# Performance work log

Measured on AMD Instinct MI355X. Metric: run time of the kernel, lower is better.

The kernel has to match this reference:

```python
import jax, jax.numpy as jnp
import numpy as np
from jax import lax

W_MAX = 8
STEP = 1
LEAK = 2
KSIZE = (W_MAX - 1) * (STEP + LEAK)  # 21 = kernel size, padding, and fodep
THETA = 80
FODEP = KSIZE
OUT_CH = 1
NEURONS = 1024


def make_w_kernel_table():
    # StepFireLeak response table: [w_max, ksize], flipped in time
    w_idx = np.arange(W_MAX, dtype=np.float32)[:, None]
    t_idx = np.arange(KSIZE, dtype=np.float32)[None, :]
    w_step = np.maximum(np.floor(1.0 + t_idx / STEP), 0.0)
    w_leak = np.maximum(np.ceil(w_idx + ((w_idx - 1.0) * STEP - t_idx) / LEAK), 0.0)
    table = np.minimum(w_step, w_leak).astype(np.int32)[:, ::-1]
    return jnp.asarray(np.ascontiguousarray(table))


def setup_inputs() -> dict:
    key = jax.random.key(0)
    k1, k2 = jax.random.split(key)
    B, C, S, T = 64, 1, 784, 500
    input_spikes = (jax.random.uniform(k1, (B, C, S, T)) < 0.05).astype(jnp.float32)
    # integer synaptic weights in [0, w_max)
    weight = jax.random.randint(k2, (OUT_CH * NEURONS, C * S), 0, W_MAX, dtype=jnp.int32)
    return {"input_spikes": input_spikes, "weight": weight}


def reference(input_spikes, weight):
    B, C, S, T = input_spikes.shape
    x = input_spikes.reshape(B, C * S, T)
    # expand integer weights into response kernels: [out, in, ksize]
    table = make_w_kernel_table().astype(jnp.float32)
    kern = table[weight]
    pot = lax.conv_general_dilated(
        x, kern, window_strides=(1,), padding=[(KSIZE, KSIZE)],
        dimension_numbers=("NCH", "OIH", "NCH"))
    pot = jnp.rint(pot).astype(jnp.int32)
    Tp = pot.shape[-1]  # T + ksize + 1
    pot = pot.reshape(B, OUT_CH, NEURONS, Tp)
    pot_t = jnp.transpose(pot, (3, 0, 1, 2))  # [Tp, B, C, N]

    def step(dep, p):  # dep: [B, C] int32, p: [B, C, N]
        winner = jnp.argmax(p, axis=-1)  # [B, C]
        val = jnp.take_along_axis(p, winner[..., None], axis=-1)[..., 0]
        cond = ((val > THETA) & (dep == 0)).astype(jnp.int32)  # min_depression == 0
        winners_t = jax.nn.one_hot(winner, NEURONS, dtype=jnp.int32) * cond[..., None]
        new_dep = jnp.maximum(0, dep + cond * (FODEP + 1) - 1)
        return new_dep, winners_t

    dep0 = jnp.zeros((B, OUT_CH), dtype=jnp.int32)
    _, winners = lax.scan(step, dep0, pot_t)  # [Tp, B, C, N]
    return jnp.transpose(winners, (1, 2, 3, 0))  # [B, C, N, Tp]
```

## Files before the change

kernel.cpp:

```cpp
#include <hip/hip_runtime.h>

#define B_DIM 64
#define S_DIM 784
#define T_DIM 500
#define N_DIM 1024
#define TP    522
#define KS    21
#define THETA 80
#define NCHUNK 8
#define CH    66
#define LISTCAP 128

__global__ void k_prep(const int* __restrict__ w, unsigned char* __restrict__ wt9,
                       unsigned* __restrict__ gcnt) {
  unsigned idx = blockIdx.x * 256 + threadIdx.x;
  if (idx < S_DIM * N_DIM) {
    unsigned s = idx >> 10, n = idx & 1023;
    int wv = w[n * S_DIM + s];
    wt9[idx] = wv ? (unsigned char)(9 * (wv - 1)) : (unsigned char)63;
  }
  if (idx < B_DIM * T_DIM) gcnt[idx] = 0;
}

__global__ void k_lists(const float* __restrict__ x, unsigned* __restrict__ gcnt,
                        unsigned short* __restrict__ glist) {
  unsigned idx = blockIdx.x * 256 + threadIdx.x;
  if (idx >= B_DIM * S_DIM * T_DIM) return;
  if (x[idx] != 0.0f) {
    unsigned t = idx % T_DIM;
    unsigned s = (idx / T_DIM) % S_DIM;
    unsigned b = idx / (S_DIM * T_DIM);
    unsigned cell = b * T_DIM + t;
    unsigned pos = atomicAdd(&gcnt[cell], 1u);
    if (pos < LISTCAP) glist[cell * LISTCAP + pos] = (unsigned short)s;
  }
}

__global__ void __launch_bounds__(1024, 8)
k_main(const unsigned char* __restrict__ wt9,
       const unsigned* __restrict__ gcnt,
       const unsigned short* __restrict__ glist,
       unsigned* __restrict__ red) {
  __shared__ unsigned short s_list[87][LISTCAP];
  __shared__ int s_cnt[87];
  __shared__ unsigned smax[CH];

  const int tid = threadIdx.x;
  const int b = blockIdx.y;
  const int lo = blockIdx.x * CH;
  const int hi = min(TP - 1, lo + CH - 1);
  const int t0 = max(0, lo - KS);
  const int n_emit = hi - lo + 1;
  const int nt_in = min(hi, T_DIM - 1) - t0 + 1;

  const unsigned cell0 = (unsigned)b * T_DIM + (unsigned)t0;
  for (int i = tid; i < nt_in; i += 1024)
    s_cnt[i] = min((int)gcnt[cell0 + i], LISTCAP);
  {
    const unsigned* src = (const unsigned*)(glist + (size_t)cell0 * LISTCAP);
    unsigned* dst = (unsigned*)&s_list[0][0];
    const int nw = nt_in * (LISTCAP / 2);
    for (int i = tid; i < nw; i += 1024) dst[i] = src[i];
  }
  for (int i = tid; i < n_emit; i += 1024) smax[i] = 0u;
  __syncthreads();

  int ring[KS + 1];
  #pragma unroll
  for (int i = 0; i <= KS; ++i) ring[i] = 0;

  const unsigned invn = (unsigned)(1023 - tid);

  for (int t = t0; t <= hi; ++t) {
    if (t >= lo) {
      unsigned key = ((unsigned)ring[0] << 10) | invn;
      #pragma unroll
      for (int off = 32; off > 0; off >>= 1) {
        unsigned o = __shfl_xor(key, off, 64);
        key = key > o ? key : o;
      }
      if ((tid & 63) == 0) atomicMax(&smax[t - lo], key);
    }

    if (t < T_DIM) {
      const int li = t - t0;
      const int cnt = __builtin_amdgcn_readfirstlane(s_cnt[li]);
      const unsigned short* lp = &s_list[li][0];
      unsigned long long ca = 0, cb = 0;
      int i = 0;
      for (; i + 1 < cnt; i += 2) {
        unsigned ia = ((unsigned)lp[i] << 10) + tid;
        unsigned ib = ((unsigned)lp[i + 1] << 10) + tid;
        ca += 1ull << wt9[ia];
        cb += 1ull << wt9[ib];
      }
      if (i < cnt) ca += 1ull << wt9[((unsigned)lp[i] << 10) + tid];
      const unsigned long long c = ca + cb;

      const int c1 = (int)(c & 511), c2 = (int)((c >> 9) & 511), c3 = (int)((c >> 18) & 511),
                c4 = (int)((c >> 27) & 511), c5 = (int)((c >> 36) & 511),
                c6 = (int)((c >> 45) & 511), c7 = (int)((c >> 54) & 511);
      const int S7 = c7, S6 = S7 + c6, S5 = S6 + c5, S4 = S5 + c4,
                S3 = S4 + c3, S2 = S3 + c2, S1 = S2 + c1;
      const int O1 = c1, O3 = O1 + c3, O5 = O3 + c5, O7 = O5 + c7;
      const int E2 = c2, E4 = E2 + c4, E6 = E4 + c6;
      const int O31 = O3 - O1, O51 = O5 - O1, O71 = O7 - O1,
                O73 = O7 - O3, O75 = O7 - O5;
      const int E62 = E6 - E2, E64 = E6 - E4;
      int acc = S1;        ring[1]  += acc;
      acc += S2;           ring[2]  += acc;
      acc += S3 - O1;      ring[3]  += acc;
      acc += S4 - E2;      ring[4]  += acc;
      acc += S5 - O31;     ring[5]  += acc;
      acc += S6 - E4;      ring[6]  += acc;
      acc += S7 - O51;     ring[7]  += acc;
      acc -= E62;          ring[8]  += acc;
      acc -= O71;          ring[9]  += acc;
      acc -= E62;          ring[10] += acc;
      acc -= O73;          ring[11] += acc;
      acc -= E62;          ring[12] += acc;
      acc -= O73;          ring[13] += acc;
      acc -= E64;          ring[14] += acc;
      acc -= O73;          ring[15] += acc;
      acc -= E64;          ring[16] += acc;
      acc -= O75;          ring[17] += acc;
      acc -= E64;          ring[18] += acc;
      acc -= O75;          ring[19] += acc;
                           ring[20] += acc;
      acc -= O75;          ring[21] += acc;
    }

    #pragma unroll
    for (int i = 0; i < KS; ++i) ring[i] = ring[i + 1];
    ring[KS] = 0;
  }

  __syncthreads();
  for (int i = tid; i < n_emit; i += 1024)
    red[(unsigned)b * TP + (unsigned)(lo + i)] = smax[i];
}

__global__ void k_scan(const unsigned* __restrict__ red, int* __restrict__ out) {
  int b = threadIdx.x;
  if (b >= B_DIM) return;
  int dep = 0;
  for (int base = 0; base < TP; base += 6) {
    unsigned buf[6];
    #pragma unroll
    for (int k = 0; k < 6; ++k) buf[k] = red[b * TP + base + k];
    #pragma unroll
    for (int k = 0; k < 6; ++k) {
      unsigned key = buf[k];
      int val = (int)(key >> 10);
      bool cond = (val > THETA) && (dep == 0);
      if (cond) {
        int idx = 1023 - (int)(key & 1023);
        out[(b * N_DIM + idx) * TP + base + k] = 1;
        dep = 22;
      }
      dep = max(0, dep - 1);
    }
  }
}

extern "C" void kernel_launch(void* const* d_in, const int* in_sizes, int n_in,
                              void* d_out, int out_size, void* d_ws, size_t ws_size,
                              hipStream_t stream) {
  const float* x = (const float*)d_in[0];
  const int* wgt = (const int*)d_in[1];
  int* out = (int*)d_out;

  unsigned char* wt9    = (unsigned char*)d_ws;
  unsigned* gcnt        = (unsigned*)((char*)d_ws + 802816);
  unsigned short* glist = (unsigned short*)((char*)d_ws + 930816);
  unsigned* red         = (unsigned*)((char*)d_ws + 9122816);

  hipMemsetAsync(d_out, 0, (size_t)out_size * sizeof(int), stream);
  k_prep<<<3136, 256, 0, stream>>>(wgt, wt9, gcnt);
  k_lists<<<(B_DIM * S_DIM * T_DIM + 255) / 256, 256, 0, stream>>>(x, gcnt, glist);
  k_main<<<dim3(NCHUNK, B_DIM), 1024, 0, stream>>>(wt9, gcnt, glist, red);
  k_scan<<<1, 64, 0, stream>>>(red, out);
}
```

Measured before the change: 686.7 us.

## Replace global atomic spike lists with ballot-built bitmaps decoded in shared memory

The per-(batch,time) spike lists built with global atomics are replaced by a bitmap kernel that uses wave ballots to pack spike bits, transposed so each time step holds 13 64-bit words over the input index. The main kernel then decodes these words into its shared-memory lists with shared atomics and ctz loops. This removes the global atomic contention, the gcnt zeroing, and the large list traffic. In exchange the order of entries within each list becomes nondeterministic and k_main gains a decode phase.

```diff
diff --git a/kernel.cpp b/kernel.cpp
--- a/kernel.cpp
+++ b/kernel.cpp
@@ -10,36 +10,51 @@
 #define NCHUNK 8
 #define CH    66
 #define LISTCAP 128
-
-__global__ void k_prep(const int* __restrict__ w, unsigned char* __restrict__ wt9,
-                       unsigned* __restrict__ gcnt) {
+#define SW64  13
+#define BMSTRIDE 16
+
+__global__ void k_prep(const int* __restrict__ w, unsigned char* __restrict__ wt9) {
   unsigned idx = blockIdx.x * 256 + threadIdx.x;
   if (idx < S_DIM * N_DIM) {
     unsigned s = idx >> 10, n = idx & 1023;
     int wv = w[n * S_DIM + s];
     wt9[idx] = wv ? (unsigned char)(9 * (wv - 1)) : (unsigned char)63;
   }
-  if (idx < B_DIM * T_DIM) gcnt[idx] = 0;
-}
-
-__global__ void k_lists(const float* __restrict__ x, unsigned* __restrict__ gcnt,
-                        unsigned short* __restrict__ glist) {
-  unsigned idx = blockIdx.x * 256 + threadIdx.x;
-  if (idx >= B_DIM * S_DIM * T_DIM) return;
-  if (x[idx] != 0.0f) {
-    unsigned t = idx % T_DIM;
-    unsigned s = (idx / T_DIM) % S_DIM;
-    unsigned b = idx / (S_DIM * T_DIM);
-    unsigned cell = b * T_DIM + t;
-    unsigned pos = atomicAdd(&gcnt[cell], 1u);
-    if (pos < LISTCAP) glist[cell * LISTCAP + pos] = (unsigned short)s;
+}
+
+__global__ void __launch_bounds__(1024)
+k_bitmap(const float* __restrict__ x, unsigned long long* __restrict__ bm) {
+  __shared__ unsigned long long s_m[S_DIM];
+  const int tid = threadIdx.x;
+  const int wave = tid >> 6, lane = tid & 63;
+  const int b = blockIdx.y;
+  const int t0 = blockIdx.x * 64;
+  const int t = t0 + lane;
+  const bool tok = (t < T_DIM);
+  const float* xb = x + (size_t)b * S_DIM * T_DIM;
+
+  for (int s = wave; s < S_DIM; s += 16) {
+    float v = tok ? xb[(size_t)s * T_DIM + t] : 0.0f;
+    unsigned long long m = __ballot(v != 0.0f);
+    if (lane == 0) s_m[s] = m;
+  }
+  __syncthreads();
+
+  if (wave < SW64) {
+    const int sbase = wave * 64;
+    const unsigned long long mask_s =
+        (sbase + lane < S_DIM) ? s_m[sbase + lane] : 0ull;
+    unsigned long long* dst = bm + ((size_t)b * 512 + t0) * BMSTRIDE + wave;
+    for (int tl = 0; tl < 64; ++tl) {
+      unsigned long long wrd = __ballot((mask_s >> tl) & 1ull);
+      if (lane == 0) dst[(size_t)tl * BMSTRIDE] = wrd;
+    }
   }
 }
 
 __global__ void __launch_bounds__(1024, 8)
 k_main(const unsigned char* __restrict__ wt9,
-       const unsigned* __restrict__ gcnt,
-       const unsigned short* __restrict__ glist,
+       const unsigned long long* __restrict__ bm,
        unsigned* __restrict__ red) {
   __shared__ unsigned short s_list[87][LISTCAP];
   __shared__ int s_cnt[87];
@@ -53,16 +68,28 @@
   const int n_emit = hi - lo + 1;
   const int nt_in = min(hi, T_DIM - 1) - t0 + 1;
 
-  const unsigned cell0 = (unsigned)b * T_DIM + (unsigned)t0;
-  for (int i = tid; i < nt_in; i += 1024)
-    s_cnt[i] = min((int)gcnt[cell0 + i], LISTCAP);
-  {
-    const unsigned* src = (const unsigned*)(glist + (size_t)cell0 * LISTCAP);
-    unsigned* dst = (unsigned*)&s_list[0][0];
-    const int nw = nt_in * (LISTCAP / 2);
-    for (int i = tid; i < nw; i += 1024) dst[i] = src[i];
-  }
+  for (int i = tid; i < nt_in; i += 1024) s_cnt[i] = 0;
   for (int i = tid; i < n_emit; i += 1024) smax[i] = 0u;
+  __syncthreads();
+
+  const unsigned long long* bmb = bm + ((size_t)b * 512 + t0) * BMSTRIDE;
+  const int ntask = nt_in * SW64;
+  for (int task = tid; task < ntask; task += 1024) {
+    const int li = task / SW64;
+    const int sw = task - li * SW64;
+    unsigned long long w = bmb[(size_t)li * BMSTRIDE + sw];
+    if (w) {
+      int c = __popcll(w);
+      int pos = atomicAdd(&s_cnt[li], c);
+      const int sb = sw * 64;
+      while (w) {
+        int j = __builtin_ctzll(w);
+        if (pos < LISTCAP) s_list[li][pos] = (unsigned short)(sb + j);
+        ++pos;
+        w &= (w - 1);
+      }
+    }
+  }
   __syncthreads();
 
   int ring[KS + 1];
@@ -84,7 +111,7 @@
 
     if (t < T_DIM) {
       const int li = t - t0;
-      const int cnt = __builtin_amdgcn_readfirstlane(s_cnt[li]);
+      const int cnt = __builtin_amdgcn_readfirstlane(min(s_cnt[li], LISTCAP));
       const unsigned short* lp = &s_list[li][0];
       unsigned long long ca = 0, cb = 0;
       int i = 0;
@@ -170,14 +197,13 @@
   const int* wgt = (const int*)d_in[1];
   int* out = (int*)d_out;
 
-  unsigned char* wt9    = (unsigned char*)d_ws;
-  unsigned* gcnt        = (unsigned*)((char*)d_ws + 802816);
-  unsigned short* glist = (unsigned short*)((char*)d_ws + 930816);
-  unsigned* red         = (unsigned*)((char*)d_ws + 9122816);
+  unsigned char* wt9      = (unsigned char*)d_ws;
+  unsigned long long* bm  = (unsigned long long*)((char*)d_ws + 802816);
+  unsigned* red           = (unsigned*)((char*)d_ws + 802816 + 4194304);
 
   hipMemsetAsync(d_out, 0, (size_t)out_size * sizeof(int), stream);
-  k_prep<<<3136, 256, 0, stream>>>(wgt, wt9, gcnt);
-  k_lists<<<(B_DIM * S_DIM * T_DIM + 255) / 256, 256, 0, stream>>>(x, gcnt, glist);
-  k_main<<<dim3(NCHUNK, B_DIM), 1024, 0, stream>>>(wt9, gcnt, glist, red);
+  k_prep<<<3136, 256, 0, stream>>>(wgt, wt9);
+  k_bitmap<<<dim3(8, B_DIM), 1024, 0, stream>>>(x, bm);
+  k_main<<<dim3(NCHUNK, B_DIM), 1024, 0, stream>>>(wt9, bm, red);
   k_scan<<<1, 64, 0, stream>>>(red, out);
 }
```

Measured after the change: 612.7 us. 1.12x faster.
